# Kernel tuning notes

Hardware: AMD Instinct MI355X
Metric: run time of the kernel (lower is better)

The kernel has to match this reference:

```python
import jax, jax.numpy as jnp
import numpy as np

ROPE_BASE = 1024.0
EPS = 1e-6

def _rms_norm(x):
    return x / jnp.sqrt(jnp.mean(x * x, axis=-1, keepdims=True) + EPS)

def _rotary_tables(T, head_dim):
    steps = head_dim // 4
    inv_freq = (1.0 / ROPE_BASE) ** jnp.linspace(0.0, 1.0, steps, dtype=jnp.float32)
    inv_freq = jnp.concatenate([inv_freq, jnp.zeros(steps, dtype=jnp.float32)])  # [head_dim//2]
    theta = jnp.arange(T, dtype=jnp.float32)[:, None] * inv_freq[None, :]  # [T, head_dim//2]
    return jnp.cos(theta), jnp.sin(theta)

def _apply_rotary(x, cos, sin):
    # x: [B,H,T,hd]; cos/sin: [T, hd//2]
    d = x.shape[-1] // 2
    x1, x2 = x[..., :d], x[..., d:]
    return jnp.concatenate([x1 * cos + x2 * sin, -x1 * sin + x2 * cos], axis=-1)

def setup_inputs() -> dict:
    key = jax.random.key(0)
    ks = jax.random.split(key, 5)
    B, T, C = 4, 2048, 1024
    return {
        "x": jax.random.normal(ks[0], (B, T, C), dtype=jnp.float32),
        "v1": jax.random.normal(ks[1], (B, T, C), dtype=jnp.float32),
        "qkv_weight": 0.02 * jax.random.normal(ks[2], (3, C, C), dtype=jnp.float32),
        "c_proj_w": 0.02 * jax.random.normal(ks[3], (C, C), dtype=jnp.float32),
        "c_proj_b": jnp.zeros((C,), dtype=jnp.float32),
        "lamb": jnp.full((1,), 0.5, dtype=jnp.float32),
        "attn_window": 512,
    }

def reference(x, v1, qkv_weight, c_proj_w, c_proj_b, lamb, attn_window):
    B, T, C = x.shape
    H = 16
    hd = C // H
    # fused QKV projection: qkv_weight is [3, C, C], applied as x @ W_k^T
    qkv = jnp.einsum('btc,kdc->kbtd', x, qkv_weight)  # [3,B,T,C]
    q, k, v = qkv[0], qkv[1], qkv[2]
    def to_heads(t):
        return t.reshape(B, T, H, hd).transpose(0, 2, 1, 3)  # [B,H,T,hd]
    query, key_, value = to_heads(q), to_heads(k), to_heads(v)
    v1h = to_heads(v1)
    lam = lamb[0]
    value = (1.0 - lam) * value + lam * v1h  # value-residual blend
    query = _rms_norm(query)
    key_ = _rms_norm(key_)
    cos, sin = _rotary_tables(T, hd)
    query = _apply_rotary(query, cos, sin)
    key_ = _apply_rotary(key_, cos, sin)
    # windowed causal mask: attend iff 0 <= i - j < attn_window
    i = jnp.arange(T)[:, None]
    j = jnp.arange(T)[None, :]
    allowed = (i - j < attn_window) & (j <= i)
    bias = jnp.where(allowed, 0.0, -jnp.inf).astype(x.dtype)  # [T,T]
    scale = 1.0 / jnp.sqrt(jnp.asarray(hd, dtype=x.dtype))
    scores = jnp.einsum('bhtd,bhsd->bhts', query, key_) * scale + bias
    attn = jax.nn.softmax(scores, axis=-1)
    out = jnp.einsum('bhts,bhsd->bhtd', attn, value)  # [B,H,T,hd]
    out = out.transpose(0, 2, 1, 3).reshape(B, T, C)
    y = out @ c_proj_w.T + c_proj_b
    return (y, value)
```

## Files before the change

kernel.cpp:

```cpp
#include <hip/hip_runtime.h>
#include <stdint.h>

typedef __attribute__((ext_vector_type(8))) short short8;
typedef __attribute__((ext_vector_type(4))) float f32x4;

#define LDS_AS __attribute__((address_space(3)))
#define GLOB_AS __attribute__((address_space(1)))

__device__ __forceinline__ void gload_lds16(const void* g, void* l) {
    __builtin_amdgcn_global_load_lds((const GLOB_AS uint32_t*)g,
                                     (LDS_AS uint32_t*)l, 16, 0, 0);
}

__device__ __forceinline__ unsigned short f2bf(float f) {
    uint32_t u = __builtin_bit_cast(uint32_t, f);
    u += 0x7fffu + ((u >> 16) & 1u);
    return (unsigned short)(u >> 16);
}
__device__ __forceinline__ float bf2f(unsigned short u) {
    uint32_t v = ((uint32_t)u) << 16;
    return __builtin_bit_cast(float, v);
}

__global__ void cvt_kernel(const float* __restrict__ src,
                           unsigned short* __restrict__ dst, int n) {
    int i = (blockIdx.x * blockDim.x + threadIdx.x) * 4;
    if (i < n) {
        float4 v = *(const float4*)(src + i);
        ushort4 o;
        o.x = f2bf(v.x); o.y = f2bf(v.y); o.z = f2bf(v.z); o.w = f2bf(v.w);
        *(ushort4*)(dst + i) = o;
    }
}

__global__ void rope_tables(float* __restrict__ cosT, float* __restrict__ sinT) {
    int tid = blockIdx.x * blockDim.x + threadIdx.x;
    int t = tid >> 5, i = tid & 31;
    float f = (i < 16) ? exp2f(-10.0f * (float)i / 15.0f) : 0.0f;
    float th = (float)t * f;
    cosT[tid] = cosf(th);
    sinT[tid] = sinf(th);
}

template <int MODE>
__global__ __launch_bounds__(256, 3) void gemm_bt(
    const unsigned short* __restrict__ A, const unsigned short* __restrict__ B,
    int K,
    unsigned short* __restrict__ qbuf, unsigned short* __restrict__ kbuf,
    float* __restrict__ vout, const float* __restrict__ v1,
    const float* __restrict__ lambp,
    float* __restrict__ y, const float* __restrict__ bias,
    const float* __restrict__ cosT, const float* __restrict__ sinT)
{
    __shared__ unsigned short As[2][128 * 32];
    __shared__ unsigned short Bs[2][128 * 32];
    const int tid = threadIdx.x;
    const int lane = tid & 63, w = tid >> 6;
    const int wr = w >> 1, wc = w & 1;
    const int lr = lane & 15, lh = lane >> 4;
    const long m0 = (long)blockIdx.x * 128;
    const long n0 = (long)blockIdx.y * 128;

    const int row0 = w * 16 + (lane >> 2);
    const int colb = (lane & 3) * 16;
    const char* pa0 = (const char*)A + ((m0 + row0) * (long)K) * 2 + colb;
    const char* pa1 = pa0 + 64 * (long)K * 2;
    const char* pb0 = (const char*)B + ((n0 + row0) * (long)K) * 2 + colb;
    const char* pb1 = pb0 + 64 * (long)K * 2;
    char* la = (char*)&As[0][0] + w * 1024;
    char* lb = (char*)&Bs[0][0] + w * 1024;
    const int BUF = 128 * 32 * 2;

    f32x4 acc[4][4] = {};

    auto STAGE = [&](int bo) {
        gload_lds16(pa0, la + bo);
        gload_lds16(pa1, la + bo + 4096);
        gload_lds16(pb0, lb + bo);
        gload_lds16(pb1, lb + bo + 4096);
        pa0 += 64; pa1 += 64; pb0 += 64; pb1 += 64;
    };
    auto COMPUTE = [&](int bo) {
        const unsigned short* as = (const unsigned short*)((const char*)&As[0][0] + bo);
        const unsigned short* bs = (const unsigned short*)((const char*)&Bs[0][0] + bo);
        short8 a[4], b[4];
        #pragma unroll
        for (int i = 0; i < 4; ++i)
            a[i] = *(const short8*)&as[(wr * 64 + i * 16 + lr) * 32 + lh * 8];
        #pragma unroll
        for (int i = 0; i < 4; ++i)
            b[i] = *(const short8*)&bs[(wc * 64 + i * 16 + lr) * 32 + lh * 8];
        #pragma unroll
        for (int i = 0; i < 4; ++i)
            #pragma unroll
            for (int j = 0; j < 4; ++j)
                acc[i][j] = __builtin_amdgcn_mfma_f32_16x16x32_bf16(
                    a[i], b[j], acc[i][j], 0, 0, 0);
    };

    STAGE(0);
    __syncthreads();
    for (int k0 = 0; k0 < K; k0 += 64) {
        STAGE(BUF);
        COMPUTE(0);
        __syncthreads();
        if (k0 + 64 < K) STAGE(0);
        COMPUTE(BUF);
        __syncthreads();
    }

    if constexpr (MODE == 1) {
        const long nbase = n0 + wc * 64;
        const int kk = (int)(nbase >> 10);
        const int h = (int)((nbase & 1023) >> 6);
        if (kk == 2) {
            float lam = lambp[0];
            #pragma unroll
            for (int i = 0; i < 4; ++i)
            #pragma unroll
            for (int j = 0; j < 4; ++j)
            #pragma unroll
            for (int r = 0; r < 4; ++r) {
                long m = m0 + wr * 64 + i * 16 + lh * 4 + r;
                long n = nbase + j * 16 + lr;
                int rem = (int)(n & 1023);
                int d = rem & 63;
                long b_ = m >> 11, t = m & 2047;
                size_t idx = (((size_t)(b_ * 16 + (rem >> 6))) * 2048 + t) * 64 + d;
                float vv = v1[(size_t)m * 1024 + rem];
                vout[idx] = (1.0f - lam) * acc[i][j][r] + lam * vv;
            }
        } else {
            unsigned short* dst = (kk == 0) ? qbuf : kbuf;
            #pragma unroll
            for (int i = 0; i < 4; ++i)
            #pragma unroll
            for (int r = 0; r < 4; ++r) {
                float v0 = acc[i][0][r], v1_ = acc[i][1][r];
                float v2 = acc[i][2][r], v3 = acc[i][3][r];
                float ss = v0 * v0 + v1_ * v1_ + v2 * v2 + v3 * v3;
                ss += __shfl_xor(ss, 1);
                ss += __shfl_xor(ss, 2);
                ss += __shfl_xor(ss, 4);
                ss += __shfl_xor(ss, 8);
                float inv = rsqrtf(ss * (1.0f / 64.0f) + 1e-6f);
                float x0 = v0 * inv, x1 = v1_ * inv;
                float x2 = v2 * inv, x3 = v3 * inv;
                long m = m0 + wr * 64 + i * 16 + lh * 4 + r;
                int t = (int)(m & 2047);
                long b_ = m >> 11;
                float c0 = cosT[t * 32 + lr],      s0 = sinT[t * 32 + lr];
                float c1 = cosT[t * 32 + 16 + lr], s1 = sinT[t * 32 + 16 + lr];
                size_t rb = (((size_t)(b_ * 16 + h)) * 2048 + t) * 64;
                dst[rb + 0 * 16 + lr] = f2bf( x0 * c0 + x2 * s0);
                dst[rb + 1 * 16 + lr] = f2bf( x1 * c1 + x3 * s1);
                dst[rb + 2 * 16 + lr] = f2bf(-x0 * s0 + x2 * c0);
                dst[rb + 3 * 16 + lr] = f2bf(-x1 * s1 + x3 * c1);
            }
        }
    } else {
        #pragma unroll
        for (int i = 0; i < 4; ++i)
        #pragma unroll
        for (int j = 0; j < 4; ++j)
        #pragma unroll
        for (int r = 0; r < 4; ++r) {
            long m = m0 + wr * 64 + i * 16 + lh * 4 + r;
            long n = n0 + wc * 64 + j * 16 + lr;
            y[(size_t)m * 1024 + n] = acc[i][j][r] + bias[n];
        }
    }
}

__global__ __launch_bounds__(256, 2) void attn_kernel(
    const unsigned short* __restrict__ qn, const unsigned short* __restrict__ kn,
    const float* __restrict__ vout, unsigned short* __restrict__ attn_out,
    const int* __restrict__ winp)
{
    __shared__ unsigned short Vt[64][72];
    __shared__ unsigned short Pl[4][16][72];
    const int tid = threadIdx.x, lane = tid & 63, w = tid >> 6;
    const int lr = lane & 15, lh = lane >> 4;
    const int bh = blockIdx.x;
    const int qt = blockIdx.y;
    const int t0 = qt * 64;
    const int win = winp[0];
    const int qrow = t0 + w * 16;

    short8 qf[2];
    #pragma unroll
    for (int ks = 0; ks < 2; ++ks)
        qf[ks] = *(const short8*)&qn[((size_t)bh * 2048 + qrow + lr) * 64 + ks * 32 + lh * 8];

    f32x4 oacc[4] = {};
    float mrow[4], lrow[4];
    #pragma unroll
    for (int r = 0; r < 4; ++r) { mrow[r] = -1e30f; lrow[r] = 0.f; }

    int kvt0 = max(0, t0 - win + 1) >> 6;
    for (int kvt = kvt0; kvt <= qt; ++kvt) {
        int j0 = kvt * 64;
        __syncthreads();
        {
            int rr = tid >> 2, c0 = (tid & 3) * 16;
            const float* src = &vout[((size_t)bh * 2048 + j0 + rr) * 64 + c0];
            #pragma unroll
            for (int jj = 0; jj < 4; ++jj) {
                float4 f = *(const float4*)(src + jj * 4);
                Vt[c0 + jj * 4 + 0][rr] = f2bf(f.x);
                Vt[c0 + jj * 4 + 1][rr] = f2bf(f.y);
                Vt[c0 + jj * 4 + 2][rr] = f2bf(f.z);
                Vt[c0 + jj * 4 + 3][rr] = f2bf(f.w);
            }
        }
        __syncthreads();

        float sv[4][4];
        #pragma unroll
        for (int kt = 0; kt < 4; ++kt) {
            f32x4 s = {};
            #pragma unroll
            for (int ks = 0; ks < 2; ++ks) {
                short8 kf = *(const short8*)&kn[((size_t)bh * 2048 + j0 + kt * 16 + lr) * 64 + ks * 32 + lh * 8];
                s = __builtin_amdgcn_mfma_f32_16x16x32_bf16(qf[ks], kf, s, 0, 0, 0);
            }
            #pragma unroll
            for (int r = 0; r < 4; ++r) {
                int qi = qrow + lh * 4 + r;
                int ji = j0 + kt * 16 + lr;
                bool ok = (ji <= qi) && (qi - ji < win);
                sv[kt][r] = ok ? s[r] * 0.125f : -1e30f;
            }
        }

        float pn[4][4];
        #pragma unroll
        for (int r = 0; r < 4; ++r) {
            float tm = fmaxf(fmaxf(sv[0][r], sv[1][r]), fmaxf(sv[2][r], sv[3][r]));
            #pragma unroll
            for (int m = 1; m < 16; m <<= 1) tm = fmaxf(tm, __shfl_xor(tm, m));
            float nm = fmaxf(mrow[r], tm);
            float alpha = __expf(mrow[r] - nm);
            float ps = 0.f;
            #pragma unroll
            for (int kt = 0; kt < 4; ++kt) {
                float p = __expf(sv[kt][r] - nm);
                pn[kt][r] = p; ps += p;
            }
            #pragma unroll
            for (int m = 1; m < 16; m <<= 1) ps += __shfl_xor(ps, m);
            lrow[r] = lrow[r] * alpha + ps;
            mrow[r] = nm;
            #pragma unroll
            for (int dt = 0; dt < 4; ++dt) oacc[dt][r] *= alpha;
        }

        #pragma unroll
        for (int kt = 0; kt < 4; ++kt)
            #pragma unroll
            for (int r = 0; r < 4; ++r)
                Pl[w][lh * 4 + r][kt * 16 + lr] = f2bf(pn[kt][r]);

        short8 pf[2];
        #pragma unroll
        for (int ks = 0; ks < 2; ++ks)
            pf[ks] = *(const short8*)&Pl[w][lr][ks * 32 + lh * 8];
        #pragma unroll
        for (int dt = 0; dt < 4; ++dt)
            #pragma unroll
            for (int ks = 0; ks < 2; ++ks) {
                short8 vf = *(const short8*)&Vt[dt * 16 + lr][ks * 32 + lh * 8];
                oacc[dt] = __builtin_amdgcn_mfma_f32_16x16x32_bf16(pf[ks], vf, oacc[dt], 0, 0, 0);
            }
    }

    int b = bh >> 4, h = bh & 15;
    #pragma unroll
    for (int dt = 0; dt < 4; ++dt)
        #pragma unroll
        for (int r = 0; r < 4; ++r) {
            int t = qrow + lh * 4 + r;
            float o = oacc[dt][r] / lrow[r];
            attn_out[((size_t)b * 2048 + t) * 1024 + h * 64 + dt * 16 + lr] = f2bf(o);
        }
}

extern "C" void kernel_launch(void* const* d_in, const int* in_sizes, int n_in,
                              void* d_out, int out_size, void* d_ws, size_t ws_size,
                              hipStream_t stream) {
    const float* x    = (const float*)d_in[0];
    const float* v1   = (const float*)d_in[1];
    const float* qkvw = (const float*)d_in[2];
    const float* cpw  = (const float*)d_in[3];
    const float* cpb  = (const float*)d_in[4];
    const float* lamb = (const float*)d_in[5];
    const int*   winp = (const int*)d_in[6];

    float* y    = (float*)d_out;
    float* vout = y + (size_t)8192 * 1024;

    char* ws = (char*)d_ws;
    unsigned short* xb   = (unsigned short*)(ws);
    unsigned short* Wb   = (unsigned short*)(ws + (16u << 20));
    unsigned short* Wp   = (unsigned short*)(ws + (22u << 20));
    unsigned short* qbuf = (unsigned short*)(ws + (24u << 20));
    unsigned short* kbuf = (unsigned short*)(ws + (40u << 20));
    float* cosT = (float*)(ws + (56u << 20));
    float* sinT = (float*)(ws + (56u << 20) + (256u << 10));

    cvt_kernel<<<8388608 / 1024, 256, 0, stream>>>(x, xb, 8388608);
    cvt_kernel<<<3145728 / 1024, 256, 0, stream>>>(qkvw, Wb, 3145728);
    cvt_kernel<<<1048576 / 1024, 256, 0, stream>>>(cpw, Wp, 1048576);
    rope_tables<<<65536 / 256, 256, 0, stream>>>(cosT, sinT);

    gemm_bt<1><<<dim3(64, 24), 256, 0, stream>>>(xb, Wb, 1024,
        qbuf, kbuf, vout, v1, lamb, nullptr, nullptr, cosT, sinT);

    attn_kernel<<<dim3(64, 32), 256, 0, stream>>>(qbuf, kbuf, vout, xb, winp);

    gemm_bt<2><<<dim3(64, 8), 256, 0, stream>>>(xb, Wp, 1024,
        nullptr, nullptr, nullptr, nullptr, nullptr, y, cpb, nullptr, nullptr);
}
```

Baseline: 215.8 us.

## Stage K and pre-transposed bf16 V through double-buffered LDS in attention

The QKV GEMM epilogue now also writes a transposed bf16 copy of V ([bh][d][t]) into the y output buffer as scratch, before y is overwritten by the projection. The attention kernel uses 512 threads covering 128 query rows and double-buffers K and V^T tiles into swizzled LDS with async global_load_lds. This replaces per-iteration fp32 V loads, scalar transposes and direct global K reads, and lets two query tiles share each KV tile. It also switches softmax to exp2 with a folded log2e scale. The extra strided bf16 V^T stores in the GEMM epilogue are uncoalesced, and waves whose rows fall outside the window sit idle while still joining every barrier.

```diff
diff --git a/kernel.cpp b/kernel.cpp
--- a/kernel.cpp
+++ b/kernel.cpp
@@ -47,8 +47,8 @@
     const unsigned short* __restrict__ A, const unsigned short* __restrict__ B,
     int K,
     unsigned short* __restrict__ qbuf, unsigned short* __restrict__ kbuf,
-    float* __restrict__ vout, const float* __restrict__ v1,
-    const float* __restrict__ lambp,
+    float* __restrict__ vout, unsigned short* __restrict__ vbT,
+    const float* __restrict__ v1, const float* __restrict__ lambp,
     float* __restrict__ y, const float* __restrict__ bias,
     const float* __restrict__ cosT, const float* __restrict__ sinT)
 {
@@ -122,13 +122,14 @@
             #pragma unroll
             for (int r = 0; r < 4; ++r) {
                 long m = m0 + wr * 64 + i * 16 + lh * 4 + r;
-                long n = nbase + j * 16 + lr;
-                int rem = (int)(n & 1023);
-                int d = rem & 63;
+                int d = j * 16 + lr;
+                int rem = h * 64 + d;
                 long b_ = m >> 11, t = m & 2047;
-                size_t idx = (((size_t)(b_ * 16 + (rem >> 6))) * 2048 + t) * 64 + d;
+                size_t idx = (((size_t)(b_ * 16 + h)) * 2048 + t) * 64 + d;
                 float vv = v1[(size_t)m * 1024 + rem];
-                vout[idx] = (1.0f - lam) * acc[i][j][r] + lam * vv;
+                float val = (1.0f - lam) * acc[i][j][r] + lam * vv;
+                vout[idx] = val;
+                vbT[(((size_t)(b_ * 16 + h)) * 64 + d) * 2048 + t] = f2bf(val);
             }
         } else {
             unsigned short* dst = (kk == 0) ? qbuf : kbuf;
@@ -172,18 +173,19 @@
     }
 }
 
-__global__ __launch_bounds__(256, 2) void attn_kernel(
+__global__ __launch_bounds__(512, 2) void attn_kernel(
     const unsigned short* __restrict__ qn, const unsigned short* __restrict__ kn,
-    const float* __restrict__ vout, unsigned short* __restrict__ attn_out,
+    const unsigned short* __restrict__ vtb, unsigned short* __restrict__ attn_out,
     const int* __restrict__ winp)
 {
-    __shared__ unsigned short Vt[64][72];
-    __shared__ unsigned short Pl[4][16][72];
+    __shared__ unsigned short Ks[2][64 * 64];
+    __shared__ unsigned short Vt[2][64 * 64];
+    __shared__ unsigned short Pl[8][16 * 72];
     const int tid = threadIdx.x, lane = tid & 63, w = tid >> 6;
     const int lr = lane & 15, lh = lane >> 4;
     const int bh = blockIdx.x;
-    const int qt = blockIdx.y;
-    const int t0 = qt * 64;
+    const int qt2 = blockIdx.y;
+    const int t0 = qt2 * 128;
     const int win = winp[0];
     const int qrow = t0 + w * 16;
 
@@ -192,86 +194,101 @@
     for (int ks = 0; ks < 2; ++ks)
         qf[ks] = *(const short8*)&qn[((size_t)bh * 2048 + qrow + lr) * 64 + ks * 32 + lh * 8];
 
+    const int srow = tid >> 3;
+    const int scol = (tid & 7) ^ (srow & 7);
+    const char* kg = (const char*)kn + ((size_t)bh * 2048 + srow) * 128 + scol * 16;
+    const char* vg = (const char*)vtb + ((size_t)(bh * 64 + srow)) * 4096 + scol * 16;
+    char* lk = (char*)&Ks[0][0] + w * 1024;
+    char* lv = (char*)&Vt[0][0] + w * 1024;
+
+    auto STAGE = [&](int buf, int j0) {
+        gload_lds16(kg + (size_t)j0 * 128, lk + buf * 8192);
+        gload_lds16(vg + (size_t)j0 * 2,   lv + buf * 8192);
+    };
+
     f32x4 oacc[4] = {};
     float mrow[4], lrow[4];
     #pragma unroll
     for (int r = 0; r < 4; ++r) { mrow[r] = -1e30f; lrow[r] = 0.f; }
 
-    int kvt0 = max(0, t0 - win + 1) >> 6;
-    for (int kvt = kvt0; kvt <= qt; ++kvt) {
-        int j0 = kvt * 64;
-        __syncthreads();
-        {
-            int rr = tid >> 2, c0 = (tid & 3) * 16;
-            const float* src = &vout[((size_t)bh * 2048 + j0 + rr) * 64 + c0];
-            #pragma unroll
-            for (int jj = 0; jj < 4; ++jj) {
-                float4 f = *(const float4*)(src + jj * 4);
-                Vt[c0 + jj * 4 + 0][rr] = f2bf(f.x);
-                Vt[c0 + jj * 4 + 1][rr] = f2bf(f.y);
-                Vt[c0 + jj * 4 + 2][rr] = f2bf(f.z);
-                Vt[c0 + jj * 4 + 3][rr] = f2bf(f.w);
+    const float C = 0.125f * 1.44269504f;
+    const int kvt0 = max(0, t0 - win + 1) >> 6;
+    const int kvt1 = (t0 + 127) >> 6;
+
+    STAGE(0, kvt0 * 64);
+    __syncthreads();
+    for (int kvt = kvt0; kvt <= kvt1; ++kvt) {
+        const int j0 = kvt * 64;
+        const int buf = (kvt - kvt0) & 1;
+        if (kvt < kvt1) STAGE(buf ^ 1, j0 + 64);
+
+        if (j0 <= qrow + 15 && j0 + 63 >= qrow + 16 - win) {
+            const char* ksb = (const char*)&Ks[buf][0];
+            const char* vtb_ = (const char*)&Vt[buf][0];
+
+            float sv[4][4];
+            #pragma unroll
+            for (int kt = 0; kt < 4; ++kt) {
+                f32x4 s = {};
+                #pragma unroll
+                for (int ks = 0; ks < 2; ++ks) {
+                    int row = kt * 16 + lr;
+                    int off = row * 128 + (((ks * 4 + lh) ^ (row & 7)) * 16);
+                    short8 kf = *(const short8*)(ksb + off);
+                    s = __builtin_amdgcn_mfma_f32_16x16x32_bf16(qf[ks], kf, s, 0, 0, 0);
+                }
+                #pragma unroll
+                for (int r = 0; r < 4; ++r) {
+                    int qi = qrow + lh * 4 + r;
+                    int ji = j0 + kt * 16 + lr;
+                    bool ok = (ji <= qi) && (qi - ji < win);
+                    sv[kt][r] = ok ? s[r] * C : -1e30f;
+                }
             }
+
+            float pn[4][4];
+            #pragma unroll
+            for (int r = 0; r < 4; ++r) {
+                float tm = fmaxf(fmaxf(sv[0][r], sv[1][r]), fmaxf(sv[2][r], sv[3][r]));
+                #pragma unroll
+                for (int m = 1; m < 16; m <<= 1) tm = fmaxf(tm, __shfl_xor(tm, m));
+                float nm = fmaxf(mrow[r], tm);
+                float alpha = exp2f(mrow[r] - nm);
+                float ps = 0.f;
+                #pragma unroll
+                for (int kt = 0; kt < 4; ++kt) {
+                    float p = exp2f(sv[kt][r] - nm);
+                    pn[kt][r] = p; ps += p;
+                }
+                #pragma unroll
+                for (int m = 1; m < 16; m <<= 1) ps += __shfl_xor(ps, m);
+                lrow[r] = lrow[r] * alpha + ps;
+                mrow[r] = nm;
+                #pragma unroll
+                for (int dt = 0; dt < 4; ++dt) oacc[dt][r] *= alpha;
+            }
+
+            #pragma unroll
+            for (int kt = 0; kt < 4; ++kt)
+                #pragma unroll
+                for (int r = 0; r < 4; ++r)
+                    Pl[w][(lh * 4 + r) * 72 + kt * 16 + lr] = f2bf(pn[kt][r]);
+
+            short8 pf[2];
+            #pragma unroll
+            for (int ks = 0; ks < 2; ++ks)
+                pf[ks] = *(const short8*)&Pl[w][lr * 72 + ks * 32 + lh * 8];
+            #pragma unroll
+            for (int dt = 0; dt < 4; ++dt)
+                #pragma unroll
+                for (int ks = 0; ks < 2; ++ks) {
+                    int row = dt * 16 + lr;
+                    int off = row * 128 + (((ks * 4 + lh) ^ (row & 7)) * 16);
+                    short8 vf = *(const short8*)(vtb_ + off);
+                    oacc[dt] = __builtin_amdgcn_mfma_f32_16x16x32_bf16(pf[ks], vf, oacc[dt], 0, 0, 0);
+                }
         }
         __syncthreads();
-
-        float sv[4][4];
-        #pragma unroll
-        for (int kt = 0; kt < 4; ++kt) {
-            f32x4 s = {};
-            #pragma unroll
-            for (int ks = 0; ks < 2; ++ks) {
-                short8 kf = *(const short8*)&kn[((size_t)bh * 2048 + j0 + kt * 16 + lr) * 64 + ks * 32 + lh * 8];
-                s = __builtin_amdgcn_mfma_f32_16x16x32_bf16(qf[ks], kf, s, 0, 0, 0);
-            }
-            #pragma unroll
-            for (int r = 0; r < 4; ++r) {
-                int qi = qrow + lh * 4 + r;
-                int ji = j0 + kt * 16 + lr;
-                bool ok = (ji <= qi) && (qi - ji < win);
-                sv[kt][r] = ok ? s[r] * 0.125f : -1e30f;
-            }
-        }
-
-        float pn[4][4];
-        #pragma unroll
-        for (int r = 0; r < 4; ++r) {
-            float tm = fmaxf(fmaxf(sv[0][r], sv[1][r]), fmaxf(sv[2][r], sv[3][r]));
-            #pragma unroll
-            for (int m = 1; m < 16; m <<= 1) tm = fmaxf(tm, __shfl_xor(tm, m));
-            float nm = fmaxf(mrow[r], tm);
-            float alpha = __expf(mrow[r] - nm);
-            float ps = 0.f;
-            #pragma unroll
-            for (int kt = 0; kt < 4; ++kt) {
-                float p = __expf(sv[kt][r] - nm);
-                pn[kt][r] = p; ps += p;
-            }
-            #pragma unroll
-            for (int m = 1; m < 16; m <<= 1) ps += __shfl_xor(ps, m);
-            lrow[r] = lrow[r] * alpha + ps;
-            mrow[r] = nm;
-            #pragma unroll
-            for (int dt = 0; dt < 4; ++dt) oacc[dt][r] *= alpha;
-        }
-
-        #pragma unroll
-        for (int kt = 0; kt < 4; ++kt)
-            #pragma unroll
-            for (int r = 0; r < 4; ++r)
-                Pl[w][lh * 4 + r][kt * 16 + lr] = f2bf(pn[kt][r]);
-
-        short8 pf[2];
-        #pragma unroll
-        for (int ks = 0; ks < 2; ++ks)
-            pf[ks] = *(const short8*)&Pl[w][lr][ks * 32 + lh * 8];
-        #pragma unroll
-        for (int dt = 0; dt < 4; ++dt)
-            #pragma unroll
-            for (int ks = 0; ks < 2; ++ks) {
-                short8 vf = *(const short8*)&Vt[dt * 16 + lr][ks * 32 + lh * 8];
-                oacc[dt] = __builtin_amdgcn_mfma_f32_16x16x32_bf16(pf[ks], vf, oacc[dt], 0, 0, 0);
-            }
     }
 
     int b = bh >> 4, h = bh & 15;
@@ -299,6 +316,8 @@
     float* y    = (float*)d_out;
     float* vout = y + (size_t)8192 * 1024;
 
+    unsigned short* vbT = (unsigned short*)y;
+
     char* ws = (char*)d_ws;
     unsigned short* xb   = (unsigned short*)(ws);
     unsigned short* Wb   = (unsigned short*)(ws + (16u << 20));
@@ -314,10 +333,10 @@
     rope_tables<<<65536 / 256, 256, 0, stream>>>(cosT, sinT);
 
     gemm_bt<1><<<dim3(64, 24), 256, 0, stream>>>(xb, Wb, 1024,
-        qbuf, kbuf, vout, v1, lamb, nullptr, nullptr, cosT, sinT);
-
-    attn_kernel<<<dim3(64, 32), 256, 0, stream>>>(qbuf, kbuf, vout, xb, winp);
+        qbuf, kbuf, vout, vbT, v1, lamb, nullptr, nullptr, cosT, sinT);
+
+    attn_kernel<<<dim3(64, 16), 512, 0, stream>>>(qbuf, kbuf, vbT, xb, winp);
 
     gemm_bt<2><<<dim3(64, 8), 256, 0, stream>>>(xb, Wp, 1024,
-        nullptr, nullptr, nullptr, nullptr, nullptr, y, cpb, nullptr, nullptr);
-}
+        nullptr, nullptr, nullptr, nullptr, nullptr, nullptr, y, cpb, nullptr, nullptr);
+}
```

After: 202.3 us. 6.2% less time.
